# Performance work log

Measured on AMD Instinct MI355X. Metric: run time of the kernel, lower is better.

## Reference

```python
import jax, jax.numpy as jnp
import numpy as np

BN, DIM, HI, WI = 1, 192, 48, 48
E, N, P, HH = 384, 16, 64, 6      # d_inner, d_state, headdim, n_heads
HALF = N // 2                      # complex state pairs
K = 4                              # cross-scan directions
L = HI * WI


def _silu(v):
    return v * jax.nn.sigmoid(v)


def _rms(v, eps=1e-6):
    return v * jax.lax.rsqrt(jnp.mean(v * v, -1, keepdims=True) + eps)


def _mamba3(x, w_zx, w_bc, b_bc, w_dt, dt_bias, A_log, theta, D_skip, rms_w, w_mout):
    # x: (BK, L, E). Mamba3 core: no conv1d, rope-factored complex SSM,
    # trapezoidal discretization, qk-normed B/C, internal silu gate + gated RMSNorm.
    BK = x.shape[0]
    zx = x @ w_zx
    z, xi = zx[..., :E], zx[..., E:]
    bc = x @ w_bc + b_bc                                   # bc_bias
    Bm, Cm = _rms(bc[..., :N]), _rms(bc[..., N:])          # qk_norm
    dt = jax.nn.softplus(x @ w_dt + dt_bias)               # (BK,L,HH)
    r = jnp.exp(-dt * jnp.exp(A_log))                      # real decay per head
    ang = jnp.cumsum(dt, 1)[..., None] * theta             # (BK,L,HH,HALF) cumulative rope angle
    c, s = jnp.cos(ang), jnp.sin(ang)

    def rot(v):  # rotate state pairs by -ang (rope factoring of complex eigenvalues)
        vp = v.reshape(BK, -1, 1, HALF, 2)
        v0, v1 = vp[..., 0], vp[..., 1]
        return jnp.stack([v0 * c + v1 * s, -v0 * s + v1 * c], -1).reshape(BK, -1, HH, N)

    Bt, Ct = rot(Bm), rot(Cm)
    xh = xi.reshape(BK, -1, HH, P)
    u = jnp.einsum('blhn,blhp->blhnp', Bt, xh)             # (BK,L,HH,N,P)
    u_prev = jnp.pad(u[:, :-1], ((0, 0), (1, 0), (0, 0), (0, 0), (0, 0)))
    # trapezoidal rule: h_t = r_t h_{t-1} + dt_t/2 (B_t x_t + r_t B_{t-1} x_{t-1})
    inp = 0.5 * dt[..., None, None] * (u + r[..., None, None] * u_prev)

    def step(h, t):
        inp_t, r_t, C_t = t
        h = r_t[..., None, None] * h + inp_t
        return h, jnp.einsum('bhn,bhnp->bhp', C_t, h)

    h0 = jnp.zeros((BK, HH, N, P), x.dtype)
    _, ys = jax.lax.scan(step, h0, (inp.transpose(1, 0, 2, 3, 4), r.transpose(1, 0, 2), Ct.transpose(1, 0, 2, 3)))
    y = ys.transpose(1, 0, 2, 3) + D_skip[None, None, :, None] * xh
    y = y.reshape(BK, -1, E)
    g = _rms(y * _silu(z)) * rms_w                          # gated RMSNorm
    return g @ w_mout


def _forward(x, w_in, w_zx, w_bc, b_bc, w_dt, dt_bias, A_log, theta, D_skip, rms_w, w_mout, w_out, ln_g, ln_b, res_scale):
    Bn = x.shape[0]
    d0 = x.reshape(Bn, DIM, L)
    d1 = jnp.swapaxes(x, 2, 3).reshape(Bn, DIM, L)
    xs = jnp.stack([d0, d1, d0[..., ::-1], d1[..., ::-1]], 1)   # (B,4,C,L) cross-scan
    x_seq = xs.reshape(Bn * K, L, DIM)                          # matches torch .view memory reinterpret
    proj = x_seq @ w_in
    x_ssm, x_gate = proj[..., :E], proj[..., E:]
    x_ssm = _mamba3(_silu(x_ssm), w_zx, w_bc, b_bc, w_dt, dt_bias, A_log, theta, D_skip, rms_w, w_mout)
    x_out = x_ssm * _silu(x_gate)                               # (BK,L,E)
    yf = jnp.swapaxes(x_out, 1, 2).reshape(Bn, K, E, L)
    m1 = jnp.swapaxes(yf[:, 1].reshape(Bn, E, WI, HI), 2, 3).reshape(Bn, E, L)
    m3 = jnp.swapaxes(yf[:, 3, :, ::-1].reshape(Bn, E, WI, HI), 2, 3).reshape(Bn, E, L)
    merged = yf[:, 0] + m1 + yf[:, 2, :, ::-1] + m3             # cross-merge
    merged = merged.reshape(Bn, E, HI, WI)
    out = jnp.einsum('behw,ed->bdhw', merged, w_out)            # 1x1 conv out_proj
    out = jnp.moveaxis(out, 1, -1)
    mu = jnp.mean(out, -1, keepdims=True)
    var = jnp.mean((out - mu) ** 2, -1, keepdims=True)
    out = (out - mu) * jax.lax.rsqrt(var + 1e-5) * ln_g + ln_b  # LayerNorm
    out = jnp.moveaxis(out, -1, 1)
    return x + res_scale[0] * out


def setup_inputs() -> dict:
    key = jax.random.key(0)
    ks = jax.random.split(key, 16)
    f = jax.random.normal
    return {
        'x': f(ks[0], (BN, DIM, HI, WI), jnp.float32),
        'w_in': f(ks[1], (DIM, 2 * E)) * 0.05,
        'w_zx': f(ks[2], (E, 2 * E)) * 0.05,
        'w_bc': f(ks[3], (E, 2 * N)) * 0.05,
        'b_bc': f(ks[4], (2 * N,)) * 0.05,
        'w_dt': f(ks[5], (E, HH)) * 0.05,
        'dt_bias': f(ks[6], (HH,)) * 0.5,
        'A_log': f(ks[7], (HH,)) * 0.5,
        'theta': f(ks[8], (HH, HALF)),
        'D_skip': f(ks[9], (HH,)) * 0.5,
        'rms_w': jnp.ones((E,)),
        'w_mout': f(ks[10], (E, E)) * 0.05,
        'w_out': f(ks[11], (E, DIM)) * 0.05,
        'ln_g': jnp.ones((DIM,)),
        'ln_b': jnp.zeros((DIM,)),
        'res_scale': jnp.full((1,), 0.5),
    }


def reference(x, w_in, w_zx, w_bc, b_bc, w_dt, dt_bias, A_log, theta, D_skip, rms_w, w_mout, w_out, ln_g, ln_b, res_scale):
    return _forward(x, w_in, w_zx, w_bc, b_bc, w_dt, dt_bias, A_log, theta, D_skip, rms_w, w_mout, w_out, ln_g, ln_b, res_scale)
```

## Files before the change

### kernel.cpp

```cpp
#include <hip/hip_runtime.h>
#include <hip/hip_bf16.h>
#include <math.h>

#define BN   1
#define DIMC 192
#define HI   48
#define WI   48
#define LL   2304
#define EE   384
#define NN   16
#define PP   64
#define HHH  6
#define HALF 8
#define KK   4
#define BK_SEQ (BN*KK)
#define NBH  (BK_SEQ*HHH)
#define CLEN 24
#define NCHUNK 96
#define ZLD  896

typedef __attribute__((ext_vector_type(8))) short bf16x8;
typedef __attribute__((ext_vector_type(4))) float f32x4;

static __device__ __forceinline__ float siluf(float v) {
    return v / (1.f + expf(-v));
}
static __device__ __forceinline__ unsigned short f2bf(float f) {
    unsigned int u = __float_as_uint(f);
    u = (u + 0x7FFFu + ((u >> 16) & 1u)) >> 16;
    return (unsigned short)u;
}
static __device__ __forceinline__ float bf2f(unsigned short u) {
    return __uint_as_float((unsigned int)u << 16);
}

#define NP0 (KK*LL*DIMC)
#define NP1 (768*DIMC)
#define NP2 (ZLD*EE)
#define NP2b 896
#define NP3 (EE*EE)
#define NP4 (256*EE)
#define NPTOT (NP0+NP1+NP2+NP2b+NP3+NP4)

__global__ __launch_bounds__(256) void k_prep_all(const float* __restrict__ x,
                                                  const float* __restrict__ w_in,
                                                  const float* __restrict__ w_zx,
                                                  const float* __restrict__ w_bc,
                                                  const float* __restrict__ w_dt,
                                                  const float* __restrict__ b_bc,
                                                  const float* __restrict__ dt_bias,
                                                  const float* __restrict__ w_mout,
                                                  const float* __restrict__ w_out,
                                                  unsigned short* __restrict__ xseq,
                                                  unsigned short* __restrict__ winT,
                                                  unsigned short* __restrict__ wcatT,
                                                  float* __restrict__ biascat,
                                                  unsigned short* __restrict__ wmoT,
                                                  unsigned short* __restrict__ woT) {
    int idx = blockIdx.x * 256 + threadIdx.x;
    if (idx < NP0) {
        int d = idx % DIMC;
        int l = (idx / DIMC) % LL;
        int k = idx / (DIMC * LL);
        int dim = l / 12;
        int pos = (l % 12) * DIMC + d;
        int src;
        if (k == 0)      src = pos;
        else if (k == 1) src = (pos % 48) * 48 + pos / 48;
        else if (k == 2) src = 2303 - pos;
        else { int p2 = 2303 - pos; src = (p2 % 48) * 48 + p2 / 48; }
        xseq[idx] = f2bf(x[dim * LL + src]);
        return;
    }
    idx -= NP0;
    if (idx < NP1) {
        int r = idx % DIMC;
        int c = idx / DIMC;
        winT[idx] = f2bf(w_in[(size_t)r * 768 + c]);
        return;
    }
    idx -= NP1;
    if (idx < NP2) {
        int n = idx / EE, k = idx % EE;
        float v = 0.f;
        if (n < 768)      v = w_zx[(size_t)k * 768 + n];
        else if (n < 800) v = w_bc[(size_t)k * 32 + (n - 768)];
        else if (n < 806) v = w_dt[(size_t)k * 6 + (n - 800)];
        wcatT[idx] = f2bf(v);
        return;
    }
    idx -= NP2;
    if (idx < NP2b) {
        float v = 0.f;
        if (idx >= 768 && idx < 800) v = b_bc[idx - 768];
        else if (idx >= 800 && idx < 806) v = dt_bias[idx - 800];
        biascat[idx] = v;
        return;
    }
    idx -= NP2b;
    if (idx < NP3) {
        int r = idx % EE;
        int c = idx / EE;
        wmoT[idx] = f2bf(w_mout[(size_t)r * EE + c]);
        return;
    }
    idx -= NP3;
    if (idx < NP4) {
        int d = idx / EE, e = idx % EE;
        woT[idx] = (d < DIMC) ? f2bf(w_out[(size_t)e * DIMC + d]) : (unsigned short)0;
    }
}

template <int EPI>
__global__ __launch_bounds__(256) void gemm_bf16(const unsigned short* __restrict__ A,
                                                 const unsigned short* __restrict__ BT,
                                                 const float* __restrict__ bias,
                                                 float* __restrict__ C,
                                                 unsigned short* __restrict__ X,
                                                 unsigned short* __restrict__ Y,
                                                 int K, int lda, int ldbt, int ldc) {
    __shared__ __align__(16) unsigned short As[2][64][40];
    __shared__ __align__(16) unsigned short Bs[2][128][40];
    int bm = blockIdx.y * 64, bn = blockIdx.x * 128;
    int tid = threadIdx.x;
    int lane = tid & 63, wave = tid >> 6;
    int wn = wave * 32;
    f32x4 acc[4][2];
#pragma unroll
    for (int f = 0; f < 4; f++)
#pragma unroll
        for (int g = 0; g < 2; g++) acc[f][g] = (f32x4){0.f, 0.f, 0.f, 0.f};

    int fr = lane & 15;
    int kl = (lane >> 4) * 8;

    int sr = tid >> 2;
    int sq = (tid & 3) * 8;
    const unsigned short* aptr  = A + (size_t)(bm + sr) * lda + sq;
    const unsigned short* bptr0 = BT + (size_t)(bn + sr) * ldbt + sq;
    const unsigned short* bptr1 = BT + (size_t)(bn + sr + 64) * ldbt + sq;

    uint4 pa  = *(const uint4*)aptr;
    uint4 pb0 = *(const uint4*)bptr0;
    uint4 pb1 = *(const uint4*)bptr1;
    *(uint4*)&As[0][sr][sq]      = pa;
    *(uint4*)&Bs[0][sr][sq]      = pb0;
    *(uint4*)&Bs[0][sr + 64][sq] = pb1;
    if (K > 32) {
        pa  = *(const uint4*)(aptr + 32);
        pb0 = *(const uint4*)(bptr0 + 32);
        pb1 = *(const uint4*)(bptr1 + 32);
    }
    __syncthreads();

    for (int k0 = 0; k0 < K; k0 += 32) {
        int cur = (k0 >> 5) & 1;
        bf16x8 af[4], bg[2];
#pragma unroll
        for (int f = 0; f < 4; f++) af[f] = *(const bf16x8*)&As[cur][f * 16 + fr][kl];
#pragma unroll
        for (int g = 0; g < 2; g++) bg[g] = *(const bf16x8*)&Bs[cur][wn + g * 16 + fr][kl];
        if (k0 + 32 < K) {
            *(uint4*)&As[cur ^ 1][sr][sq]      = pa;
            *(uint4*)&Bs[cur ^ 1][sr][sq]      = pb0;
            *(uint4*)&Bs[cur ^ 1][sr + 64][sq] = pb1;
        }
        if (k0 + 64 < K) {
            pa  = *(const uint4*)(aptr + k0 + 64);
            pb0 = *(const uint4*)(bptr0 + k0 + 64);
            pb1 = *(const uint4*)(bptr1 + k0 + 64);
        }
        __syncthreads();
#pragma unroll
        for (int f = 0; f < 4; f++)
#pragma unroll
            for (int g = 0; g < 2; g++)
                acc[f][g] = __builtin_amdgcn_mfma_f32_16x16x32_bf16(af[f], bg[g], acc[f][g], 0, 0, 0);
    }
    int cc = lane & 15, crb = (lane >> 4) * 4;
#pragma unroll
    for (int f = 0; f < 4; f++)
#pragma unroll
        for (int g = 0; g < 2; g++) {
            int col = bn + wn + g * 16 + cc;
            int rowb = bm + f * 16 + crb;
            if (EPI == 0) {
                float bv = bias ? bias[col] : 0.f;
#pragma unroll
                for (int i = 0; i < 4; i++)
                    C[(size_t)(rowb + i) * ldc + col] = acc[f][g][i] + bv;
            } else if (EPI == 1) {
                if (col < 384) {
#pragma unroll
                    for (int i = 0; i < 4; i++)
                        X[(size_t)(rowb + i) * 384 + col] = f2bf(siluf(acc[f][g][i]));
                } else {
#pragma unroll
                    for (int i = 0; i < 4; i++)
                        Y[(size_t)(rowb + i) * 384 + col - 384] = f2bf(siluf(acc[f][g][i]));
                }
            } else if (EPI == 2) {
                if (col < 384) {
#pragma unroll
                    for (int i = 0; i < 4; i++)
                        X[(size_t)(rowb + i) * 384 + col] = f2bf(siluf(acc[f][g][i]));
                } else if (col < 768) {
#pragma unroll
                    for (int i = 0; i < 4; i++)
                        Y[(size_t)(rowb + i) * 384 + col - 384] = f2bf(acc[f][g][i]);
                } else {
                    float bv = bias[col];
#pragma unroll
                    for (int i = 0; i < 4; i++)
                        C[(size_t)(rowb + i) * 128 + col - 768] = acc[f][g][i] + bv;
                }
            } else {
#pragma unroll
                for (int i = 0; i < 4; i++)
                    X[(size_t)(rowb + i) * ldc + col] = f2bf(acc[f][g][i]);
            }
        }
}

__global__ __launch_bounds__(256) void k_dtcum(const float* __restrict__ bcdt,
                                               const float* __restrict__ A_log,
                                               float* __restrict__ dtv,
                                               float* __restrict__ rrv,
                                               float* __restrict__ cum) {
    int bh = blockIdx.x;
    int tid = threadIdx.x;
    int b = bh / HHH, h = bh % HHH;
    float aexp = expf(A_log[h]);
    const int PER = 9;
    int base = tid * PER;
    float p[PER];
    float s = 0.f;
#pragma unroll
    for (int j = 0; j < PER; j++) {
        int l = base + j;
        float xv = bcdt[((size_t)b * LL + l) * 128 + 32 + h];
        float sp = fmaxf(xv, 0.f) + log1pf(expf(-fabsf(xv)));
        dtv[(size_t)bh * LL + l] = sp;
        rrv[(size_t)bh * LL + l] = expf(-sp * aexp);
        s += sp; p[j] = s;
    }
    __shared__ float sh[256];
    sh[tid] = s;
    __syncthreads();
    for (int off = 1; off < 256; off <<= 1) {
        float t = (tid >= off) ? sh[tid - off] : 0.f;
        __syncthreads();
        sh[tid] += t;
        __syncthreads();
    }
    float excl = sh[tid] - s;
#pragma unroll
    for (int j = 0; j < PER; j++) cum[(size_t)bh * LL + base + j] = excl + p[j];
}

__global__ __launch_bounds__(256) void k_rot(const float* __restrict__ bcdt,
                                             const float* __restrict__ cum,
                                             const float* __restrict__ theta,
                                             float* __restrict__ btct) {
    int idx = blockIdx.x * 256 + threadIdx.x;
    if (idx >= NBH * LL) return;
    int bh = idx / LL, l = idx % LL;
    int b = bh / HHH, h = bh % HHH;
    const float* bcrow = bcdt + ((size_t)b * LL + l) * 128;
    float Bm[16], Cm[16];
    float sb = 0.f, sc = 0.f;
#pragma unroll
    for (int j = 0; j < 16; j++) {
        Bm[j] = bcrow[j];      sb += Bm[j] * Bm[j];
        Cm[j] = bcrow[16 + j]; sc += Cm[j] * Cm[j];
    }
    float rb = rsqrtf(sb * (1.f / 16.f) + 1e-6f);
    float rc = rsqrtf(sc * (1.f / 16.f) + 1e-6f);
    float cd = cum[(size_t)bh * LL + l];
    float* out = btct + ((size_t)bh * LL + l) * 32;
#pragma unroll
    for (int j = 0; j < 8; j++) {
        float ang = cd * theta[h * 8 + j];
        float cc = cosf(ang), ss = sinf(ang);
        float b0 = Bm[2 * j] * rb, b1 = Bm[2 * j + 1] * rb;
        out[2 * j]     = b0 * cc + b1 * ss;
        out[2 * j + 1] = -b0 * ss + b1 * cc;
        float c0 = Cm[2 * j] * rc, c1 = Cm[2 * j + 1] * rc;
        out[16 + 2 * j]     = c0 * cc + c1 * ss;
        out[16 + 2 * j + 1] = -c0 * ss + c1 * cc;
    }
}

template <int MODE>
__global__ __launch_bounds__(64) void k_scan_phase(const float* __restrict__ btct,
                                                   const float* __restrict__ rrv,
                                                   const float* __restrict__ dtv,
                                                   const unsigned short* __restrict__ xhb,
                                                   const float* __restrict__ h0,
                                                   float* __restrict__ Hc,
                                                   float* __restrict__ Rc,
                                                   unsigned short* __restrict__ yDb,
                                                   const float* __restrict__ Dsk) {
    int chunk = blockIdx.x;
    int bh = blockIdx.y;
    int lane = threadIdx.x;
    int b = bh / HHH, h = bh % HHH;
    int t0 = chunk * CLEN;

    __shared__ float sbt[(CLEN + 1) * 32];
    __shared__ float srd[2 * CLEN];

    const float* bt_row = btct + (size_t)bh * LL * 32;
    for (int i = lane; i < (CLEN + 1) * 8; i += 64) {
        int t = t0 - 1 + (i >> 3);
        float4 v = make_float4(0.f, 0.f, 0.f, 0.f);
        if (t >= 0)
            v = ((const float4*)(bt_row + (size_t)t * 32))[i & 7];
        ((float4*)sbt)[i] = v;
    }
    if (lane < CLEN) {
        srd[lane] = rrv[(size_t)bh * LL + t0 + lane];
        srd[CLEN + lane] = 0.5f * dtv[(size_t)bh * LL + t0 + lane];
    }

    const unsigned short* xcol = xhb + (size_t)b * LL * EE + h * PP + lane;
    float xr[CLEN];
#pragma unroll
    for (int j = 0; j < CLEN; j++) xr[j] = bf2f(xcol[(size_t)(t0 + j) * EE]);
    float xprev = (t0 > 0) ? bf2f(xcol[(size_t)(t0 - 1) * EE]) : 0.f;

    float hreg[16];
    if (MODE == 0) {
#pragma unroll
        for (int n = 0; n < 16; n++) hreg[n] = 0.f;
    } else {
        const float* hp = h0 + ((size_t)(chunk * NBH + bh) * 16) * PP + lane;
#pragma unroll
        for (int n = 0; n < 16; n++) hreg[n] = hp[n * PP];
    }
    float dsk = (MODE == 1) ? Dsk[h] : 0.f;
    __syncthreads();

    float Btp[16];
#pragma unroll
    for (int n = 0; n < 16; n++) Btp[n] = sbt[n];
    float Rprod = 1.f;

#pragma unroll
    for (int j = 0; j < CLEN; j++) {
        float r = srd[j];
        float dhalf = srd[CLEN + j];
        float xcur = xr[j];
        const float* bb = sbt + (j + 1) * 32;
        float a = dhalf * xcur;
        float ap = dhalf * r * xprev;
        float y = 0.f;
#pragma unroll
        for (int n = 0; n < 16; n++) {
            float Btn = bb[n];
            hreg[n] = r * hreg[n] + a * Btn + ap * Btp[n];
            Btp[n] = Btn;
            if (MODE) y += bb[16 + n] * hreg[n];
        }
        xprev = xcur;
        if (MODE) {
            yDb[((size_t)b * LL + t0 + j) * EE + h * PP + lane] = f2bf(y + dsk * xcur);
        } else {
            Rprod *= r;
        }
    }
    if (MODE == 0) {
        float* Hp = Hc + ((size_t)(chunk * NBH + bh) * 16) * PP + lane;
#pragma unroll
        for (int n = 0; n < 16; n++) Hp[n * PP] = hreg[n];
        if (lane == 0) Rc[chunk * NBH + bh] = Rprod;
    }
}

__global__ __launch_bounds__(64) void k_scan_combine(const float* __restrict__ Hc,
                                                     const float* __restrict__ Rc,
                                                     float* __restrict__ h0) {
    int bh = blockIdx.x;
    int lane = threadIdx.x;
    float s[16];
#pragma unroll
    for (int n = 0; n < 16; n++) s[n] = 0.f;
    float* out0 = h0 + ((size_t)(0 * NBH + bh) * 16) * PP + lane;
#pragma unroll
    for (int n = 0; n < 16; n++) out0[n * PP] = 0.f;
    for (int c = 0; c < NCHUNK - 1; ++c) {
        float R = Rc[c * NBH + bh];
        const float* Hp = Hc + ((size_t)(c * NBH + bh) * 16) * PP + lane;
        float* op = h0 + ((size_t)((c + 1) * NBH + bh) * 16) * PP + lane;
#pragma unroll
        for (int n = 0; n < 16; n++) {
            s[n] = R * s[n] + Hp[n * PP];
            op[n * PP] = s[n];
        }
    }
}

__global__ __launch_bounds__(128) void k_gmul(const unsigned short* __restrict__ yDb,
                                              const unsigned short* __restrict__ zsil,
                                              const float* __restrict__ rms_w,
                                              unsigned short* __restrict__ g) {
    int row = blockIdx.x;
    int tid = threadIdx.x;
    int lane = tid & 63, wid = tid >> 6;
    float v[3];
    float ss = 0.f;
#pragma unroll
    for (int j = 0; j < 3; j++) {
        int e = tid * 3 + j;
        float y = bf2f(yDb[(size_t)row * EE + e]);
        float zs = bf2f(zsil[(size_t)row * EE + e]);
        v[j] = y * zs;
        ss += v[j] * v[j];
    }
#pragma unroll
    for (int off = 1; off < 64; off <<= 1) ss += __shfl_xor(ss, off);
    __shared__ float red[2];
    if (lane == 0) red[wid] = ss;
    __syncthreads();
    float total = red[0] + red[1];
    float scale = rsqrtf(total * (1.f / (float)EE) + 1e-6f);
#pragma unroll
    for (int j = 0; j < 3; j++) {
        int e = tid * 3 + j;
        g[(size_t)row * EE + e] = f2bf(v[j] * scale * rms_w[e]);
    }
}

__global__ __launch_bounds__(256) void k_merge(const unsigned short* __restrict__ mresb,
                                               const unsigned short* __restrict__ gsil,
                                               unsigned short* __restrict__ mrg) {
    int idx = blockIdx.x * 256 + threadIdx.x;
    if (idx >= LL * EE) return;
    int e = idx % EE, l = idx / EE;
    int l1 = (l % 48) * 48 + l / 48;
    int rows[4];
    rows[0] = 0 * LL + l;
    rows[1] = 1 * LL + l1;
    rows[2] = 2 * LL + (2303 - l);
    rows[3] = 3 * LL + (2303 - l1);
    float acc = 0.f;
#pragma unroll
    for (int k = 0; k < 4; k++) {
        float m = bf2f(mresb[(size_t)rows[k] * EE + e]);
        float gz = bf2f(gsil[(size_t)rows[k] * EE + e]);
        acc += m * gz;
    }
    mrg[idx] = f2bf(acc);
}

__global__ __launch_bounds__(64) void k_ln(const float* __restrict__ outT,
                                           const float* __restrict__ x,
                                           const float* __restrict__ ln_g,
                                           const float* __restrict__ ln_b,
                                           const float* __restrict__ res_scale,
                                           float* __restrict__ outF) {
    int l = blockIdx.x;
    int lane = threadIdx.x;
    float v[3];
    float s = 0.f;
#pragma unroll
    for (int j = 0; j < 3; j++) {
        int d = lane * 3 + j;
        v[j] = outT[(size_t)l * 256 + d];
        s += v[j];
    }
#pragma unroll
    for (int off = 1; off < 64; off <<= 1) s += __shfl_xor(s, off);
    float mu = s * (1.f / (float)DIMC);
    float sq = 0.f;
#pragma unroll
    for (int j = 0; j < 3; j++) { float dlt = v[j] - mu; sq += dlt * dlt; }
#pragma unroll
    for (int off = 1; off < 64; off <<= 1) sq += __shfl_xor(sq, off);
    float rstd = rsqrtf(sq * (1.f / (float)DIMC) + 1e-5f);
    float rs = res_scale[0];
#pragma unroll
    for (int j = 0; j < 3; j++) {
        int d = lane * 3 + j;
        outF[(size_t)d * LL + l] =
            x[(size_t)d * LL + l] + rs * ((v[j] - mu) * rstd * ln_g[d] + ln_b[d]);
    }
}

extern "C" void kernel_launch(void* const* d_in, const int* in_sizes, int n_in,
                              void* d_out, int out_size, void* d_ws, size_t ws_size,
                              hipStream_t stream) {
    const float* x        = (const float*)d_in[0];
    const float* w_in     = (const float*)d_in[1];
    const float* w_zx     = (const float*)d_in[2];
    const float* w_bc     = (const float*)d_in[3];
    const float* b_bc     = (const float*)d_in[4];
    const float* w_dt     = (const float*)d_in[5];
    const float* dt_bias  = (const float*)d_in[6];
    const float* A_log    = (const float*)d_in[7];
    const float* theta    = (const float*)d_in[8];
    const float* D_skip   = (const float*)d_in[9];
    const float* rms_w    = (const float*)d_in[10];
    const float* w_mout   = (const float*)d_in[11];
    const float* w_out    = (const float*)d_in[12];
    const float* ln_g     = (const float*)d_in[13];
    const float* ln_b     = (const float*)d_in[14];
    const float* res_scale= (const float*)d_in[15];
    float* outF = (float*)d_out;
    float* ws = (float*)d_ws;

    size_t o = 0;
    auto alloc = [&](size_t n) { size_t r = o; o += (n + 127) & ~(size_t)127; return r; };
    size_t xseqb_o = alloc((size_t)9216 * DIMC / 2);
    size_t winT_o  = alloc((size_t)768 * DIMC / 2);
    size_t wcatT_o = alloc((size_t)ZLD * EE / 2);
    size_t wmoT_o  = alloc((size_t)384 * 384 / 2);
    size_t woT_o   = alloc((size_t)256 * EE / 2);
    size_t bcat_o  = alloc(ZLD);
    size_t xact_o  = alloc((size_t)9216 * EE / 2);
    size_t gsil_o  = alloc((size_t)9216 * EE / 2);
    size_t zsil_o  = alloc((size_t)9216 * EE / 2);
    size_t xhb_o   = alloc((size_t)9216 * EE / 2);
    size_t bcdt_o  = alloc((size_t)9216 * 128);
    size_t dtv_o   = alloc((size_t)NBH * LL);
    size_t rrv_o   = alloc((size_t)NBH * LL);
    size_t cum_o   = alloc((size_t)NBH * LL);
    size_t btct_o  = alloc((size_t)NBH * LL * 32);
    size_t Hc_o    = alloc((size_t)NCHUNK * NBH * 16 * PP);
    size_t Rc_o    = alloc((size_t)NCHUNK * NBH);
    size_t h0_o    = alloc((size_t)NCHUNK * NBH * 16 * PP);
    size_t yDb_o   = alloc((size_t)9216 * EE / 2);
    size_t mrg_o   = alloc((size_t)LL * EE / 2);
    size_t outT_o  = alloc((size_t)LL * 256);

    unsigned short* xseqb = (unsigned short*)(ws + xseqb_o);
    unsigned short* winT  = (unsigned short*)(ws + winT_o);
    unsigned short* wcatT = (unsigned short*)(ws + wcatT_o);
    unsigned short* wmoT  = (unsigned short*)(ws + wmoT_o);
    unsigned short* woT   = (unsigned short*)(ws + woT_o);
    float* bcat = ws + bcat_o;
    unsigned short* xact = (unsigned short*)(ws + xact_o);
    unsigned short* gsil = (unsigned short*)(ws + gsil_o);
    unsigned short* zsil = (unsigned short*)(ws + zsil_o);
    unsigned short* xhb  = (unsigned short*)(ws + xhb_o);
    float* bcdt = ws + bcdt_o;
    float* dtv  = ws + dtv_o;
    float* rrv  = ws + rrv_o;
    float* cum  = ws + cum_o;
    float* btct = ws + btct_o;
    float* Hc   = ws + Hc_o;
    float* Rc   = ws + Rc_o;
    float* h0   = ws + h0_o;
    unsigned short* yDb = (unsigned short*)(ws + yDb_o);
    unsigned short* mrg = (unsigned short*)(ws + mrg_o);
    float* outT = ws + outT_o;
    unsigned short* g_bf  = xact;
    unsigned short* mresb = zsil;

    k_prep_all<<<(NPTOT + 255) / 256, 256, 0, stream>>>(
        x, w_in, w_zx, w_bc, w_dt, b_bc, dt_bias, w_mout, w_out,
        xseqb, winT, wcatT, bcat, wmoT, woT);
    gemm_bf16<1><<<dim3(768 / 128, 9216 / 64), 256, 0, stream>>>(
        xseqb, winT, nullptr, nullptr, xact, gsil, DIMC, DIMC, DIMC, 0);
    gemm_bf16<2><<<dim3(ZLD / 128, 9216 / 64), 256, 0, stream>>>(
        xact, wcatT, bcat, bcdt, zsil, xhb, EE, EE, EE, 0);
    k_dtcum<<<NBH, 256, 0, stream>>>(bcdt, A_log, dtv, rrv, cum);
    k_rot<<<(NBH * LL + 255) / 256, 256, 0, stream>>>(bcdt, cum, theta, btct);
    k_scan_phase<0><<<dim3(NCHUNK, NBH), 64, 0, stream>>>(btct, rrv, dtv, xhb, h0, Hc, Rc, yDb, D_skip);
    k_scan_combine<<<NBH, 64, 0, stream>>>(Hc, Rc, h0);
    k_scan_phase<1><<<dim3(NCHUNK, NBH), 64, 0, stream>>>(btct, rrv, dtv, xhb, h0, Hc, Rc, yDb, D_skip);
    k_gmul<<<9216, 128, 0, stream>>>(yDb, zsil, rms_w, g_bf);
    gemm_bf16<3><<<dim3(384 / 128, 9216 / 64), 256, 0, stream>>>(
        g_bf, wmoT, nullptr, nullptr, mresb, nullptr, 384, 384, 384, 384);
    k_merge<<<(LL * EE + 255) / 256, 256, 0, stream>>>(mresb, gsil, mrg);
    gemm_bf16<0><<<dim3(256 / 128, LL / 64), 256, 0, stream>>>(
        mrg, woT, nullptr, outT, nullptr, nullptr, EE, EE, EE, 256);
    k_ln<<<LL, 64, 0, stream>>>(outT, x, ln_g, ln_b, res_scale, outF);
    (void)in_sizes; (void)n_in; (void)out_size; (void)ws_size;
}
```

Before: 158.3 us.

## Replace two-pass chunked scan with local scan plus carry correction in gating

The second scan pass is removed. The chunk-local scan now writes y and the running within-chunk decay product directly. The incoming chunk state's contribution (Rprod_t · C_t·h0) is added later inside the gated-RMSNorm kernel. The cumsum and rope-rotation kernels are also fused into one kernel that keeps the cumulative angle in shared memory. This saves one full scan launch and its state reloads, but it runs the rotation work on only 24 blocks and adds a strided 16-term dot product per element in the gating kernel.

```diff
diff --git a/kernel.cpp b/kernel.cpp
--- a/kernel.cpp
+++ b/kernel.cpp
@@ -222,11 +222,14 @@
         }
 }
 
-__global__ __launch_bounds__(256) void k_dtcum(const float* __restrict__ bcdt,
+__global__ __launch_bounds__(256) void k_dtrot(const float* __restrict__ bcdt,
                                                const float* __restrict__ A_log,
+                                               const float* __restrict__ theta,
                                                float* __restrict__ dtv,
                                                float* __restrict__ rrv,
-                                               float* __restrict__ cum) {
+                                               float* __restrict__ btct) {
+    __shared__ float sh[256];
+    __shared__ float sh_cum[LL];
     int bh = blockIdx.x;
     int tid = threadIdx.x;
     int b = bh / HHH, h = bh % HHH;
@@ -244,7 +247,6 @@
         rrv[(size_t)bh * LL + l] = expf(-sp * aexp);
         s += sp; p[j] = s;
     }
-    __shared__ float sh[256];
     sh[tid] = s;
     __syncthreads();
     for (int off = 1; off < 256; off <<= 1) {
@@ -255,50 +257,45 @@
     }
     float excl = sh[tid] - s;
 #pragma unroll
-    for (int j = 0; j < PER; j++) cum[(size_t)bh * LL + base + j] = excl + p[j];
-}
-
-__global__ __launch_bounds__(256) void k_rot(const float* __restrict__ bcdt,
-                                             const float* __restrict__ cum,
-                                             const float* __restrict__ theta,
-                                             float* __restrict__ btct) {
-    int idx = blockIdx.x * 256 + threadIdx.x;
-    if (idx >= NBH * LL) return;
-    int bh = idx / LL, l = idx % LL;
-    int b = bh / HHH, h = bh % HHH;
-    const float* bcrow = bcdt + ((size_t)b * LL + l) * 128;
-    float Bm[16], Cm[16];
-    float sb = 0.f, sc = 0.f;
-#pragma unroll
-    for (int j = 0; j < 16; j++) {
-        Bm[j] = bcrow[j];      sb += Bm[j] * Bm[j];
-        Cm[j] = bcrow[16 + j]; sc += Cm[j] * Cm[j];
-    }
-    float rb = rsqrtf(sb * (1.f / 16.f) + 1e-6f);
-    float rc = rsqrtf(sc * (1.f / 16.f) + 1e-6f);
-    float cd = cum[(size_t)bh * LL + l];
-    float* out = btct + ((size_t)bh * LL + l) * 32;
-#pragma unroll
-    for (int j = 0; j < 8; j++) {
-        float ang = cd * theta[h * 8 + j];
-        float cc = cosf(ang), ss = sinf(ang);
-        float b0 = Bm[2 * j] * rb, b1 = Bm[2 * j + 1] * rb;
-        out[2 * j]     = b0 * cc + b1 * ss;
-        out[2 * j + 1] = -b0 * ss + b1 * cc;
-        float c0 = Cm[2 * j] * rc, c1 = Cm[2 * j + 1] * rc;
-        out[16 + 2 * j]     = c0 * cc + c1 * ss;
-        out[16 + 2 * j + 1] = -c0 * ss + c1 * cc;
-    }
-}
-
-template <int MODE>
-__global__ __launch_bounds__(64) void k_scan_phase(const float* __restrict__ btct,
+    for (int j = 0; j < PER; j++) sh_cum[base + j] = excl + p[j];
+    __syncthreads();
+
+    float th[8];
+#pragma unroll
+    for (int j = 0; j < 8; j++) th[j] = theta[h * 8 + j];
+    for (int l = tid; l < LL; l += 256) {
+        const float* bcrow = bcdt + ((size_t)b * LL + l) * 128;
+        float Bm[16], Cm[16];
+        float sb = 0.f, sc = 0.f;
+#pragma unroll
+        for (int j = 0; j < 16; j++) {
+            Bm[j] = bcrow[j];      sb += Bm[j] * Bm[j];
+            Cm[j] = bcrow[16 + j]; sc += Cm[j] * Cm[j];
+        }
+        float rb = rsqrtf(sb * (1.f / 16.f) + 1e-6f);
+        float rc = rsqrtf(sc * (1.f / 16.f) + 1e-6f);
+        float cd = sh_cum[l];
+        float* out = btct + ((size_t)bh * LL + l) * 32;
+#pragma unroll
+        for (int j = 0; j < 8; j++) {
+            float ang = cd * th[j];
+            float ccv = cosf(ang), ssv = sinf(ang);
+            float b0 = Bm[2 * j] * rb, b1 = Bm[2 * j + 1] * rb;
+            out[2 * j]     = b0 * ccv + b1 * ssv;
+            out[2 * j + 1] = -b0 * ssv + b1 * ccv;
+            float c0 = Cm[2 * j] * rc, c1 = Cm[2 * j + 1] * rc;
+            out[16 + 2 * j]     = c0 * ccv + c1 * ssv;
+            out[16 + 2 * j + 1] = -c0 * ssv + c1 * ccv;
+        }
+    }
+}
+
+__global__ __launch_bounds__(64) void k_scan_local(const float* __restrict__ btct,
                                                    const float* __restrict__ rrv,
                                                    const float* __restrict__ dtv,
                                                    const unsigned short* __restrict__ xhb,
-                                                   const float* __restrict__ h0,
                                                    float* __restrict__ Hc,
-                                                   float* __restrict__ Rc,
+                                                   float* __restrict__ RP,
                                                    unsigned short* __restrict__ yDb,
                                                    const float* __restrict__ Dsk) {
     int chunk = blockIdx.x;
@@ -330,15 +327,9 @@
     float xprev = (t0 > 0) ? bf2f(xcol[(size_t)(t0 - 1) * EE]) : 0.f;
 
     float hreg[16];
-    if (MODE == 0) {
-#pragma unroll
-        for (int n = 0; n < 16; n++) hreg[n] = 0.f;
-    } else {
-        const float* hp = h0 + ((size_t)(chunk * NBH + bh) * 16) * PP + lane;
-#pragma unroll
-        for (int n = 0; n < 16; n++) hreg[n] = hp[n * PP];
-    }
-    float dsk = (MODE == 1) ? Dsk[h] : 0.f;
+#pragma unroll
+    for (int n = 0; n < 16; n++) hreg[n] = 0.f;
+    float dsk = Dsk[h];
     __syncthreads();
 
     float Btp[16];
@@ -360,25 +351,20 @@
             float Btn = bb[n];
             hreg[n] = r * hreg[n] + a * Btn + ap * Btp[n];
             Btp[n] = Btn;
-            if (MODE) y += bb[16 + n] * hreg[n];
+            y += bb[16 + n] * hreg[n];
         }
         xprev = xcur;
-        if (MODE) {
-            yDb[((size_t)b * LL + t0 + j) * EE + h * PP + lane] = f2bf(y + dsk * xcur);
-        } else {
-            Rprod *= r;
-        }
-    }
-    if (MODE == 0) {
-        float* Hp = Hc + ((size_t)(chunk * NBH + bh) * 16) * PP + lane;
-#pragma unroll
-        for (int n = 0; n < 16; n++) Hp[n * PP] = hreg[n];
-        if (lane == 0) Rc[chunk * NBH + bh] = Rprod;
-    }
+        Rprod *= r;
+        yDb[((size_t)b * LL + t0 + j) * EE + h * PP + lane] = f2bf(y + dsk * xcur);
+        if (lane == 0) RP[(size_t)bh * LL + t0 + j] = Rprod;
+    }
+    float* Hp = Hc + ((size_t)(chunk * NBH + bh) * 16) * PP + lane;
+#pragma unroll
+    for (int n = 0; n < 16; n++) Hp[n * PP] = hreg[n];
 }
 
 __global__ __launch_bounds__(64) void k_scan_combine(const float* __restrict__ Hc,
-                                                     const float* __restrict__ Rc,
+                                                     const float* __restrict__ RP,
                                                      float* __restrict__ h0) {
     int bh = blockIdx.x;
     int lane = threadIdx.x;
@@ -389,7 +375,7 @@
 #pragma unroll
     for (int n = 0; n < 16; n++) out0[n * PP] = 0.f;
     for (int c = 0; c < NCHUNK - 1; ++c) {
-        float R = Rc[c * NBH + bh];
+        float R = RP[(size_t)bh * LL + c * CLEN + CLEN - 1];
         const float* Hp = Hc + ((size_t)(c * NBH + bh) * 16) * PP + lane;
         float* op = h0 + ((size_t)((c + 1) * NBH + bh) * 16) * PP + lane;
 #pragma unroll
@@ -402,9 +388,14 @@
 
 __global__ __launch_bounds__(128) void k_gmul(const unsigned short* __restrict__ yDb,
                                               const unsigned short* __restrict__ zsil,
+                                              const float* __restrict__ btct,
+                                              const float* __restrict__ RP,
+                                              const float* __restrict__ h0,
                                               const float* __restrict__ rms_w,
                                               unsigned short* __restrict__ g) {
     int row = blockIdx.x;
+    int b = row / LL, l = row % LL;
+    int chunk = l / CLEN;
     int tid = threadIdx.x;
     int lane = tid & 63, wid = tid >> 6;
     float v[3];
@@ -412,7 +403,15 @@
 #pragma unroll
     for (int j = 0; j < 3; j++) {
         int e = tid * 3 + j;
+        int h = e >> 6, pp = e & 63;
+        int bh = b * HHH + h;
         float y = bf2f(yDb[(size_t)row * EE + e]);
+        const float* ct = btct + ((size_t)bh * LL + l) * 32 + 16;
+        const float* h0p = h0 + ((size_t)(chunk * NBH + bh) * 16) * PP + pp;
+        float corr = 0.f;
+#pragma unroll
+        for (int n = 0; n < 16; n++) corr += ct[n] * h0p[n * PP];
+        y += RP[(size_t)bh * LL + l] * corr;
         float zs = bf2f(zsil[(size_t)row * EE + e]);
         v[j] = y * zs;
         ss += v[j] * v[j];
@@ -524,10 +523,9 @@
     size_t bcdt_o  = alloc((size_t)9216 * 128);
     size_t dtv_o   = alloc((size_t)NBH * LL);
     size_t rrv_o   = alloc((size_t)NBH * LL);
-    size_t cum_o   = alloc((size_t)NBH * LL);
+    size_t RP_o    = alloc((size_t)NBH * LL);
     size_t btct_o  = alloc((size_t)NBH * LL * 32);
     size_t Hc_o    = alloc((size_t)NCHUNK * NBH * 16 * PP);
-    size_t Rc_o    = alloc((size_t)NCHUNK * NBH);
     size_t h0_o    = alloc((size_t)NCHUNK * NBH * 16 * PP);
     size_t yDb_o   = alloc((size_t)9216 * EE / 2);
     size_t mrg_o   = alloc((size_t)LL * EE / 2);
@@ -546,10 +544,9 @@
     float* bcdt = ws + bcdt_o;
     float* dtv  = ws + dtv_o;
     float* rrv  = ws + rrv_o;
-    float* cum  = ws + cum_o;
+    float* RP   = ws + RP_o;
     float* btct = ws + btct_o;
     float* Hc   = ws + Hc_o;
-    float* Rc   = ws + Rc_o;
     float* h0   = ws + h0_o;
     unsigned short* yDb = (unsigned short*)(ws + yDb_o);
     unsigned short* mrg = (unsigned short*)(ws + mrg_o);
@@ -564,12 +561,10 @@
         xseqb, winT, nullptr, nullptr, xact, gsil, DIMC, DIMC, DIMC, 0);
     gemm_bf16<2><<<dim3(ZLD / 128, 9216 / 64), 256, 0, stream>>>(
         xact, wcatT, bcat, bcdt, zsil, xhb, EE, EE, EE, 0);
-    k_dtcum<<<NBH, 256, 0, stream>>>(bcdt, A_log, dtv, rrv, cum);
-    k_rot<<<(NBH * LL + 255) / 256, 256, 0, stream>>>(bcdt, cum, theta, btct);
-    k_scan_phase<0><<<dim3(NCHUNK, NBH), 64, 0, stream>>>(btct, rrv, dtv, xhb, h0, Hc, Rc, yDb, D_skip);
-    k_scan_combine<<<NBH, 64, 0, stream>>>(Hc, Rc, h0);
-    k_scan_phase<1><<<dim3(NCHUNK, NBH), 64, 0, stream>>>(btct, rrv, dtv, xhb, h0, Hc, Rc, yDb, D_skip);
-    k_gmul<<<9216, 128, 0, stream>>>(yDb, zsil, rms_w, g_bf);
+    k_dtrot<<<NBH, 256, 0, stream>>>(bcdt, A_log, theta, dtv, rrv, btct);
+    k_scan_local<<<dim3(NCHUNK, NBH), 64, 0, stream>>>(btct, rrv, dtv, xhb, Hc, RP, yDb, D_skip);
+    k_scan_combine<<<NBH, 64, 0, stream>>>(Hc, RP, h0);
+    k_gmul<<<9216, 128, 0, stream>>>(yDb, zsil, btct, RP, h0, rms_w, g_bf);
     gemm_bf16<3><<<dim3(384 / 128, 9216 / 64), 256, 0, stream>>>(
         g_bf, wmoT, nullptr, nullptr, mresb, nullptr, 384, 384, 384, 384);
     k_merge<<<(LL * EE + 255) / 256, 256, 0, stream>>>(mresb, gsil, mrg);
```

New measurement: 213.1 us. 34.6% more time.
